# Optimization experiments

Hardware: AMD Instinct MI355X
Metric: run time of the kernel (lower is better)

## Reference

```python
import jax, jax.numpy as jnp
import numpy as np

P = 16           # patch size
D = 768          # embed / feature dim (= 3*P*P)
T = 8            # number of task vectors
H_META = 192     # MetaNet hidden (= D // 4)


def patchify(x):
    # x: [B, 3, H, W] -> [B, N, 3*P*P]
    B, C, H, W = x.shape
    x = x.reshape(B, C, H // P, P, W // P, P)
    x = x.transpose(0, 2, 4, 1, 3, 5)
    return x.reshape(B, (H // P) * (W // P), C * P * P)


def encode(W1, b1, W2, b2, x):
    # base functional encoder f(params, x): shared weights over the batch
    patches = patchify(x)                       # [B, N, D]
    h = jax.nn.relu(patches @ W1 + b1)          # [B, N, D]
    pooled = h.mean(axis=1)                     # [B, D]
    return pooled @ W2 + b2                     # [B, D]


def setup_inputs() -> dict:
    key = jax.random.key(0)
    ks = jax.random.split(key, 14)
    B = 64
    s = 0.02
    return {
        "x":   jax.random.normal(ks[0], (B, 3, 224, 224), jnp.float32),
        # base model params
        "W1":  jax.random.normal(ks[1], (D, D), jnp.float32) * s,
        "b1":  jax.random.normal(ks[2], (D,), jnp.float32) * s,
        "W2":  jax.random.normal(ks[3], (D, D), jnp.float32) * s,
        "b2":  jax.random.normal(ks[4], (D,), jnp.float32) * s,
        # task-vector deltas (stacked over T tasks)
        "dW1": jax.random.normal(ks[5], (T, D, D), jnp.float32) * s,
        "db1": jax.random.normal(ks[6], (T, D), jnp.float32) * s,
        "dW2": jax.random.normal(ks[7], (T, D, D), jnp.float32) * s,
        "db2": jax.random.normal(ks[8], (T, D), jnp.float32) * s,
        # MetaNet (Linear-ReLU-Linear); zero-init in the original, random here
        "mw1": jax.random.normal(ks[9], (D, H_META), jnp.float32) * s,
        "mb1": jax.random.normal(ks[10], (H_META,), jnp.float32) * s,
        "mw2": jax.random.normal(ks[11], (H_META, T), jnp.float32) * s,
        "mb2": jax.random.normal(ks[12], (T,), jnp.float32) * s,
    }


def reference(x, W1, b1, W2, b2, dW1, db1, dW2, db2, mw1, mb1, mw2, mb2):
    # 1) base features with frozen base model (torch.no_grad)
    base = jax.lax.stop_gradient(encode(W1, b1, W2, b2, x))       # [B, D]
    # 2) per-sample mixing coefficients via MetaNet
    coefs = jax.nn.relu(base @ mw1 + mb1) @ mw2 + mb2             # [B, T]
    # 3) per-sample mixed parameters: p + sum_t c[b,t] * dp[t]
    nW1 = W1 + jnp.einsum("bt,tij->bij", coefs, dW1)              # [B, D, D]
    nb1 = b1 + coefs @ db1                                        # [B, D]
    nW2 = W2 + jnp.einsum("bt,tij->bij", coefs, dW2)              # [B, D, D]
    nb2 = b2 + coefs @ db2                                        # [B, D]
    # 4) batched per-sample forward with the mixed weights
    patches = patchify(x)                                         # [B, N, D]
    h = jax.nn.relu(jnp.einsum("bnd,bde->bne", patches, nW1) + nb1[:, None, :])
    pooled = h.mean(axis=1)                                       # [B, D]
    out = jnp.einsum("bd,bde->be", pooled, nW2) + nb2             # [B, D]
    return out
```

## Files before the change

### kernel.cpp

```cpp
#include <hip/hip_runtime.h>
#include <hip/hip_bf16.h>


typedef __bf16 bf16x8 __attribute__((ext_vector_type(8)));
typedef float f32x4 __attribute__((ext_vector_type(4)));
typedef __hip_bfloat16 bf16;

struct alignas(16) BF8 { bf16 h[8]; };

constexpr int BATCH = 64;
constexpr int NP    = 196;
constexpr int NPAD  = 256;
constexpr int DIM   = 768;
constexpr int NT    = 8;
constexpr size_t MSZ = (size_t)DIM * DIM;

__device__ __forceinline__ void async_cp16(const void* g, void* l) {
  __builtin_amdgcn_global_load_lds(
      (const __attribute__((address_space(1))) uint32_t*)g,
      (__attribute__((address_space(3))) uint32_t*)l, 16, 0, 0);
}

__global__ void k_patchify(const float* __restrict__ x, bf16* __restrict__ A) {
  int idx  = blockIdx.x * blockDim.x + threadIdx.x;
  int col4 = idx % (DIM / 4);
  int row  = idx / (DIM / 4);
  int d = col4 * 4;
  int b = row >> 8;
  int n = row & 255;
  bf16 tmp[4];
  if (n < NP) {
    int hp = n / 14, wp = n % 14;
    int c  = d >> 8;
    int rr = d & 255;
    int i = rr >> 4, j = rr & 15;
    const float* src = x + ((((size_t)b * 3 + c) * 224 + hp * 16 + i) * 224 + wp * 16 + j);
    float4 f = *(const float4*)src;
    tmp[0] = __float2bfloat16(f.x);
    tmp[1] = __float2bfloat16(f.y);
    tmp[2] = __float2bfloat16(f.z);
    tmp[3] = __float2bfloat16(f.w);
  } else {
    tmp[0] = tmp[1] = tmp[2] = tmp[3] = __float2bfloat16(0.0f);
  }
  *(ushort4*)(A + (size_t)row * DIM + d) = *(ushort4*)tmp;
}

__global__ void k_transpose_cast(const float* __restrict__ W1, const float* __restrict__ dW1,
                                 const float* __restrict__ W2, const float* __restrict__ dW2,
                                 bf16* __restrict__ WT) {
  __shared__ float tile[32][33];
  int mat = blockIdx.z;
  const float* src;
  if      (mat == 0) src = W1;
  else if (mat <= 8) src = dW1 + (size_t)(mat - 1) * MSZ;
  else if (mat == 9) src = W2;
  else               src = dW2 + (size_t)(mat - 10) * MSZ;
  int n0 = blockIdx.x * 32;
  int k0 = blockIdx.y * 32;
  int tx = threadIdx.x & 31, ty = threadIdx.x >> 5;
#pragma unroll
  for (int r = ty; r < 32; r += 8)
    tile[r][tx] = src[(size_t)(k0 + r) * DIM + n0 + tx];
  __syncthreads();
  bf16* dst = WT + (size_t)mat * MSZ;
#pragma unroll
  for (int r = ty; r < 32; r += 8)
    dst[(size_t)(n0 + r) * DIM + k0 + tx] = __float2bfloat16(tile[tx][r]);
}


template<int MIX>
__global__ __launch_bounds__(256, 3)
void k_gemm_pool(const bf16* __restrict__ A,
                 const bf16* __restrict__ WT,
                 const float* __restrict__ b1,
                 const float* __restrict__ db1,
                 const float* __restrict__ coefs,
                 float* __restrict__ pooled) {
  __shared__ uint4 AslU[256 * 8];
  __shared__ uint4 BslU[64 * 8];
  __shared__ float biasl[64];
  __shared__ float cl[NT];
  __shared__ float red[4][64];

  int b  = blockIdx.x;
  int n0 = blockIdx.y * 64;
  int tid = threadIdx.x;

  if (MIX) {
    if (tid < NT) cl[tid] = coefs[b * NT + tid];
    __syncthreads();
  }
  if (tid < 64) {
    float bias = b1[n0 + tid];
    if (MIX) {
#pragma unroll
      for (int t = 0; t < NT; t++) bias += cl[t] * db1[t * DIM + n0 + tid];
    }
    biasl[tid] = bias;
  }
  float cr[NT];
  if (MIX) {
#pragma unroll
    for (int t = 0; t < NT; t++) cr[t] = cl[t];
  }

  const bf16* Ag = A + (size_t)b * NPAD * DIM;
  int wave = tid >> 6, lane = tid & 63;
  int quad = lane >> 4, l16 = lane & 15;
  f32x4 acc[4][4] = {};

  for (int kt = 0; kt < 12; kt++) {
    const bf16* Ak = Ag + kt * 64;
    const bf16* Wk = WT + kt * 64;
#pragma unroll
    for (int i = 0; i < 8; i++) {
      int s = wave * 512 + i * 64 + lane;
      int r = s >> 3, c = (s & 7) ^ (r & 7);
      async_cp16(Ak + (size_t)r * DIM + c * 8, (void*)(AslU + wave * 512 + i * 64));
    }
    if (!MIX) {
#pragma unroll
      for (int i = 0; i < 2; i++) {
        int s = wave * 128 + i * 64 + lane;
        int r = s >> 3, c = (s & 7) ^ (r & 7);
        async_cp16(Wk + (size_t)(n0 + r) * DIM + c * 8, (void*)(BslU + wave * 128 + i * 64));
      }
    } else {
#pragma unroll
      for (int i = 0; i < 2; i++) {
        int g = tid + 256 * i;
        int r = g >> 3, c = (g & 7) ^ (r & 7);
        const bf16* p0 = Wk + (size_t)(n0 + r) * DIM + c * 8;
        BF8 w = *(const BF8*)p0;
        float m[8];
#pragma unroll
        for (int j = 0; j < 8; j++) m[j] = __bfloat162float(w.h[j]);
#pragma unroll
        for (int t = 0; t < NT; t++) {
          BF8 dv = *(const BF8*)(p0 + (size_t)(1 + t) * MSZ);
          float cc = cr[t];
#pragma unroll
          for (int j = 0; j < 8; j++) m[j] += cc * __bfloat162float(dv.h[j]);
        }
        BF8 o;
#pragma unroll
        for (int j = 0; j < 8; j++) o.h[j] = __float2bfloat16(m[j]);
        BslU[g] = *(uint4*)&o;
      }
    }
    __syncthreads();
    const bf16* As = (const bf16*)AslU;
    const bf16* Bs = (const bf16*)BslU;
#pragma unroll
    for (int ks = 0; ks < 2; ks++) {
      bf16x8 bfr[4];
#pragma unroll
      for (int nf = 0; nf < 4; nf++) {
        int brow = nf * 16 + l16;
        bfr[nf] = *(const bf16x8*)(Bs + ((size_t)brow * 8 + ((ks * 4 + quad) ^ (brow & 7))) * 8);
      }
#pragma unroll
      for (int mf = 0; mf < 4; mf++) {
        int arow = wave * 64 + mf * 16 + l16;
        bf16x8 af = *(const bf16x8*)(As + ((size_t)arow * 8 + ((ks * 4 + quad) ^ (arow & 7))) * 8);
#pragma unroll
        for (int nf = 0; nf < 4; nf++)
          acc[mf][nf] = __builtin_amdgcn_mfma_f32_16x16x32_bf16(af, bfr[nf], acc[mf][nf], 0, 0, 0);
      }
    }
    __syncthreads();
  }

  int m0 = wave * 64;
  float colsum[4];
#pragma unroll
  for (int nf = 0; nf < 4; nf++) {
    float bias = biasl[nf * 16 + l16];
    float s = 0.0f;
#pragma unroll
    for (int mf = 0; mf < 4; mf++) {
      int rbase = m0 + mf * 16 + quad * 4;
#pragma unroll
      for (int r = 0; r < 4; r++) {
        if (rbase + r < NP) s += fmaxf(acc[mf][nf][r] + bias, 0.0f);
      }
    }
    s += __shfl_xor(s, 16, 64);
    s += __shfl_xor(s, 32, 64);
    colsum[nf] = s;
  }
  if (lane < 16) {
#pragma unroll
    for (int nf = 0; nf < 4; nf++) red[wave][nf * 16 + lane] = colsum[nf];
  }
  __syncthreads();
  if (tid < 64) {
    float s = red[0][tid] + red[1][tid] + red[2][tid] + red[3][tid];
    pooled[(size_t)b * DIM + n0 + tid] = s * (1.0f / 196.0f);
  }
}

__global__ __launch_bounds__(256, 2)
void k_gemm2(const float* __restrict__ Af,
             const bf16* __restrict__ WT,
             int matbase,
             const float* __restrict__ bias,
             float* __restrict__ Y) {
  __shared__ uint4 AslU[64 * 8];
  __shared__ uint4 BslU[64 * 8];
  int n0  = blockIdx.x * 64;
  int mat = blockIdx.y;
  int tid = threadIdx.x, wave = tid >> 6, lane = tid & 63;
  int quad = lane >> 4, l16 = lane & 15;
  f32x4 acc[4] = {};
  const bf16* Wm = WT + (size_t)(matbase + mat) * MSZ;
  for (int k0 = 0; k0 < DIM; k0 += 64) {
#pragma unroll
    for (int i = 0; i < 2; i++) {
      int g = tid + i * 256;
      int r = g >> 3, c = g & 7;
      const float* src = Af + (size_t)r * DIM + k0 + c * 8;
      float4 xa = ((const float4*)src)[0];
      float4 xb = ((const float4*)src)[1];
      BF8 o;
      o.h[0] = __float2bfloat16(xa.x); o.h[1] = __float2bfloat16(xa.y);
      o.h[2] = __float2bfloat16(xa.z); o.h[3] = __float2bfloat16(xa.w);
      o.h[4] = __float2bfloat16(xb.x); o.h[5] = __float2bfloat16(xb.y);
      o.h[6] = __float2bfloat16(xb.z); o.h[7] = __float2bfloat16(xb.w);
      AslU[r * 8 + (c ^ (r & 7))] = *(uint4*)&o;
      BslU[r * 8 + (c ^ (r & 7))] = *(const uint4*)(Wm + (size_t)(n0 + r) * DIM + k0 + c * 8);
    }
    __syncthreads();
    const bf16* As = (const bf16*)AslU;
    const bf16* Bs = (const bf16*)BslU;
#pragma unroll
    for (int ks = 0; ks < 2; ks++) {
      int brow = wave * 16 + l16;
      bf16x8 bfr = *(const bf16x8*)(Bs + (size_t)(brow * 8 + ((ks * 4 + quad) ^ (brow & 7))) * 8);
#pragma unroll
      for (int mf = 0; mf < 4; mf++) {
        int arow = mf * 16 + l16;
        bf16x8 af = *(const bf16x8*)(As + (size_t)(arow * 8 + ((ks * 4 + quad) ^ (arow & 7))) * 8);
        acc[mf] = __builtin_amdgcn_mfma_f32_16x16x32_bf16(af, bfr, acc[mf], 0, 0, 0);
      }
    }
    __syncthreads();
  }
#pragma unroll
  for (int mf = 0; mf < 4; mf++) {
#pragma unroll
    for (int r = 0; r < 4; r++) {
      int row = mf * 16 + quad * 4 + r;
      int col = n0 + wave * 16 + l16;
      float v = acc[mf][r];
      if (bias) v += bias[col];
      Y[((size_t)mat * 64 + row) * DIM + col] = v;
    }
  }
}

__global__ void k_metanet(const float* __restrict__ base,
                          const float* __restrict__ mw1, const float* __restrict__ mb1,
                          const float* __restrict__ mw2, const float* __restrict__ mb2,
                          float* __restrict__ coefs) {
  __shared__ float bl[DIM];
  __shared__ float hl[192];
  int b = blockIdx.x, tid = threadIdx.x;
  for (int i = tid; i < DIM; i += 192) bl[i] = base[(size_t)b * DIM + i];
  __syncthreads();
  float s = mb1[tid];
  for (int k = 0; k < DIM; k++) s += bl[k] * mw1[(size_t)k * 192 + tid];
  hl[tid] = fmaxf(s, 0.0f);
  __syncthreads();
  if (tid < NT) {
    float c = mb2[tid];
    for (int j = 0; j < 192; j++) c += hl[j] * mw2[(size_t)j * NT + tid];
    coefs[b * NT + tid] = c;
  }
}

__global__ void k_combine(const float* __restrict__ Y,
                          const float* __restrict__ coefs,
                          const float* __restrict__ b2,
                          const float* __restrict__ db2,
                          float* __restrict__ out) {
  int idx = blockIdx.x * 256 + threadIdx.x;
  int b = idx / DIM, e = idx % DIM;
  float v = Y[(size_t)b * DIM + e] + b2[e];
#pragma unroll
  for (int t = 0; t < NT; t++) {
    float c = coefs[b * NT + t];
    v += c * (Y[((size_t)(1 + t) * 64 + b) * DIM + e] + db2[(size_t)t * DIM + e]);
  }
  out[idx] = v;
}

extern "C" void kernel_launch(void* const* d_in, const int* in_sizes, int n_in,
                              void* d_out, int out_size, void* d_ws, size_t ws_size,
                              hipStream_t stream) {
  const float* x   = (const float*)d_in[0];
  const float* W1  = (const float*)d_in[1];
  const float* b1  = (const float*)d_in[2];
  const float* W2  = (const float*)d_in[3];
  const float* b2  = (const float*)d_in[4];
  const float* dW1 = (const float*)d_in[5];
  const float* db1 = (const float*)d_in[6];
  const float* dW2 = (const float*)d_in[7];
  const float* db2 = (const float*)d_in[8];
  const float* mw1 = (const float*)d_in[9];
  const float* mb1 = (const float*)d_in[10];
  const float* mw2 = (const float*)d_in[11];
  const float* mb2 = (const float*)d_in[12];
  float* out = (float*)d_out;
  (void)in_sizes; (void)n_in; (void)out_size; (void)ws_size;

  char* ws = (char*)d_ws;
  bf16*  A_bf    = (bf16*) (ws);
  bf16*  WT      = (bf16*) (ws + 25165824);
  float* pooledA = (float*)(ws + 46399488);
  float* pooledB = (float*)(ws + 46596096);
  float* coefs   = (float*)(ws + 46792704);
  float* base    = (float*)(ws + 46794752);
  float* Y       = (float*)(ws + 46991360);

  k_patchify<<<dim3((BATCH * NPAD * (DIM / 4)) / 256), 256, 0, stream>>>(x, A_bf);
  k_transpose_cast<<<dim3(24, 24, 18), 256, 0, stream>>>(W1, dW1, W2, dW2, WT);
  k_gemm_pool<0><<<dim3(BATCH, DIM / 64), 256, 0, stream>>>(A_bf, WT, b1, db1, nullptr, pooledA);
  k_gemm2<<<dim3(DIM / 64, 1), 256, 0, stream>>>(pooledA, WT, 9, b2, base);
  k_metanet<<<dim3(BATCH), 192, 0, stream>>>(base, mw1, mb1, mw2, mb2, coefs);
  k_gemm_pool<1><<<dim3(BATCH, DIM / 64), 256, 0, stream>>>(A_bf, WT, b1, db1, coefs, pooledB);
  k_gemm2<<<dim3(DIM / 64, 9), 256, 0, stream>>>(pooledB, WT, 9, nullptr, Y);
  k_combine<<<dim3((BATCH * DIM) / 256), 256, 0, stream>>>(Y, coefs, b2, db2, out);
}
```

Measured before the change: 306.6 us.

## Double-buffer LDS tiles in patch GEMM and skip padded rows beyond 224

Adds double buffering to the patch-embedding GEMM+pool kernel, so the next k-tile's A and B loads (async LDS copies, or register-staged mixed weights in the MIX path) are issued before the current tile's MFMAs run. It also loads only 224 of the 256 padded A rows and skips MFMAs for the all-padding row block. The bias is computed per lane at the end instead of being staged through LDS. The doubled LDS use and the larger register set for prefetched weights lower the occupancy target from 3 to 2 blocks per CU.

After: 293.9 us. 4.2% less time.

```diff
diff --git a/kernel.cpp b/kernel.cpp
--- a/kernel.cpp
+++ b/kernel.cpp
@@ -71,88 +71,97 @@
 
 
 template<int MIX>
-__global__ __launch_bounds__(256, 3)
+__global__ __launch_bounds__(256, 2)
 void k_gemm_pool(const bf16* __restrict__ A,
                  const bf16* __restrict__ WT,
                  const float* __restrict__ b1,
                  const float* __restrict__ db1,
                  const float* __restrict__ coefs,
                  float* __restrict__ pooled) {
-  __shared__ uint4 AslU[256 * 8];
-  __shared__ uint4 BslU[64 * 8];
-  __shared__ float biasl[64];
-  __shared__ float cl[NT];
-  __shared__ float red[4][64];
+  __shared__ uint4 AslU[2][1792];
+  __shared__ uint4 BslU[2][512];
 
   int b  = blockIdx.x;
   int n0 = blockIdx.y * 64;
   int tid = threadIdx.x;
-
-  if (MIX) {
-    if (tid < NT) cl[tid] = coefs[b * NT + tid];
-    __syncthreads();
-  }
-  if (tid < 64) {
-    float bias = b1[n0 + tid];
-    if (MIX) {
-#pragma unroll
-      for (int t = 0; t < NT; t++) bias += cl[t] * db1[t * DIM + n0 + tid];
-    }
-    biasl[tid] = bias;
-  }
+  int wave = tid >> 6, lane = tid & 63;
+  int quad = lane >> 4, l16 = lane & 15;
+
   float cr[NT];
   if (MIX) {
 #pragma unroll
-    for (int t = 0; t < NT; t++) cr[t] = cl[t];
+    for (int t = 0; t < NT; t++) cr[t] = coefs[b * NT + t];
   }
 
   const bf16* Ag = A + (size_t)b * NPAD * DIM;
-  int wave = tid >> 6, lane = tid & 63;
-  int quad = lane >> 4, l16 = lane & 15;
   f32x4 acc[4][4] = {};
 
+  auto stage_a = [&](int buf, int kt) {
+    const bf16* Ak = Ag + kt * 64;
+#pragma unroll
+    for (int i = 0; i < 7; i++) {
+      int s = (wave * 7 + i) * 64 + lane;
+      int r = s >> 3, c = (s & 7) ^ (r & 7);
+      async_cp16(Ak + (size_t)r * DIM + c * 8, (void*)&AslU[buf][(wave * 7 + i) * 64]);
+    }
+  };
+  auto stage_b_async = [&](int buf, int kt) {
+    const bf16* Wk = WT + kt * 64;
+#pragma unroll
+    for (int i = 0; i < 2; i++) {
+      int s = (wave * 2 + i) * 64 + lane;
+      int r = s >> 3, c = (s & 7) ^ (r & 7);
+      async_cp16(Wk + (size_t)(n0 + r) * DIM + c * 8, (void*)&BslU[buf][(wave * 2 + i) * 64]);
+    }
+  };
+  BF8 wreg[2][9];
+  auto mixb_load = [&](int kt) {
+    const bf16* Wk = WT + kt * 64;
+#pragma unroll
+    for (int i = 0; i < 2; i++) {
+      int g = tid + 256 * i;
+      int r = g >> 3, c = (g & 7) ^ (r & 7);
+      const bf16* p0 = Wk + (size_t)(n0 + r) * DIM + c * 8;
+      wreg[i][0] = *(const BF8*)p0;
+#pragma unroll
+      for (int t = 0; t < NT; t++)
+        wreg[i][1 + t] = *(const BF8*)(p0 + (size_t)(1 + t) * MSZ);
+    }
+  };
+  auto mixb_write = [&](int buf) {
+#pragma unroll
+    for (int i = 0; i < 2; i++) {
+      int g = tid + 256 * i;
+      float m[8];
+#pragma unroll
+      for (int j = 0; j < 8; j++) m[j] = __bfloat162float(wreg[i][0].h[j]);
+#pragma unroll
+      for (int t = 0; t < NT; t++) {
+        float cc = cr[t];
+#pragma unroll
+        for (int j = 0; j < 8; j++) m[j] += cc * __bfloat162float(wreg[i][1 + t].h[j]);
+      }
+      BF8 o;
+#pragma unroll
+      for (int j = 0; j < 8; j++) o.h[j] = __float2bfloat16(m[j]);
+      BslU[buf][g] = *(uint4*)&o;
+    }
+  };
+
+  stage_a(0, 0);
+  if (MIX) { mixb_load(0); mixb_write(0); }
+  else     stage_b_async(0, 0);
+  __syncthreads();
+
+  int cur = 0;
   for (int kt = 0; kt < 12; kt++) {
-    const bf16* Ak = Ag + kt * 64;
-    const bf16* Wk = WT + kt * 64;
-#pragma unroll
-    for (int i = 0; i < 8; i++) {
-      int s = wave * 512 + i * 64 + lane;
-      int r = s >> 3, c = (s & 7) ^ (r & 7);
-      async_cp16(Ak + (size_t)r * DIM + c * 8, (void*)(AslU + wave * 512 + i * 64));
-    }
-    if (!MIX) {
-#pragma unroll
-      for (int i = 0; i < 2; i++) {
-        int s = wave * 128 + i * 64 + lane;
-        int r = s >> 3, c = (s & 7) ^ (r & 7);
-        async_cp16(Wk + (size_t)(n0 + r) * DIM + c * 8, (void*)(BslU + wave * 128 + i * 64));
-      }
-    } else {
-#pragma unroll
-      for (int i = 0; i < 2; i++) {
-        int g = tid + 256 * i;
-        int r = g >> 3, c = (g & 7) ^ (r & 7);
-        const bf16* p0 = Wk + (size_t)(n0 + r) * DIM + c * 8;
-        BF8 w = *(const BF8*)p0;
-        float m[8];
-#pragma unroll
-        for (int j = 0; j < 8; j++) m[j] = __bfloat162float(w.h[j]);
-#pragma unroll
-        for (int t = 0; t < NT; t++) {
-          BF8 dv = *(const BF8*)(p0 + (size_t)(1 + t) * MSZ);
-          float cc = cr[t];
-#pragma unroll
-          for (int j = 0; j < 8; j++) m[j] += cc * __bfloat162float(dv.h[j]);
-        }
-        BF8 o;
-#pragma unroll
-        for (int j = 0; j < 8; j++) o.h[j] = __float2bfloat16(m[j]);
-        BslU[g] = *(uint4*)&o;
-      }
-    }
-    __syncthreads();
-    const bf16* As = (const bf16*)AslU;
-    const bf16* Bs = (const bf16*)BslU;
+    if (kt < 11) {
+      stage_a(cur ^ 1, kt + 1);
+      if (MIX) mixb_load(kt + 1);
+      else     stage_b_async(cur ^ 1, kt + 1);
+    }
+    const bf16* As = (const bf16*)AslU[cur];
+    const bf16* Bs = (const bf16*)BslU[cur];
 #pragma unroll
     for (int ks = 0; ks < 2; ks++) {
       bf16x8 bfr[4];
@@ -163,21 +172,31 @@
       }
 #pragma unroll
       for (int mf = 0; mf < 4; mf++) {
-        int arow = wave * 64 + mf * 16 + l16;
-        bf16x8 af = *(const bf16x8*)(As + ((size_t)arow * 8 + ((ks * 4 + quad) ^ (arow & 7))) * 8);
-#pragma unroll
-        for (int nf = 0; nf < 4; nf++)
-          acc[mf][nf] = __builtin_amdgcn_mfma_f32_16x16x32_bf16(af, bfr[nf], acc[mf][nf], 0, 0, 0);
-      }
-    }
+        if (wave * 64 + mf * 16 < 224) {
+          int arow = wave * 64 + mf * 16 + l16;
+          bf16x8 af = *(const bf16x8*)(As + ((size_t)arow * 8 + ((ks * 4 + quad) ^ (arow & 7))) * 8);
+#pragma unroll
+          for (int nf = 0; nf < 4; nf++)
+            acc[mf][nf] = __builtin_amdgcn_mfma_f32_16x16x32_bf16(af, bfr[nf], acc[mf][nf], 0, 0, 0);
+        }
+      }
+    }
+    if (MIX && kt < 11) mixb_write(cur ^ 1);
     __syncthreads();
-  }
-
+    cur ^= 1;
+  }
+
+  float* red = (float*)&BslU[0][0];
   int m0 = wave * 64;
   float colsum[4];
 #pragma unroll
   for (int nf = 0; nf < 4; nf++) {
-    float bias = biasl[nf * 16 + l16];
+    int col = n0 + nf * 16 + l16;
+    float bias = b1[col];
+    if (MIX) {
+#pragma unroll
+      for (int t = 0; t < NT; t++) bias += cr[t] * db1[t * DIM + col];
+    }
     float s = 0.0f;
 #pragma unroll
     for (int mf = 0; mf < 4; mf++) {
@@ -193,11 +212,11 @@
   }
   if (lane < 16) {
 #pragma unroll
-    for (int nf = 0; nf < 4; nf++) red[wave][nf * 16 + lane] = colsum[nf];
+    for (int nf = 0; nf < 4; nf++) red[wave * 64 + nf * 16 + lane] = colsum[nf];
   }
   __syncthreads();
   if (tid < 64) {
-    float s = red[0][tid] + red[1][tid] + red[2][tid] + red[3][tid];
+    float s = red[tid] + red[64 + tid] + red[128 + tid] + red[192 + tid];
     pooled[(size_t)b * DIM + n0 + tid] = s * (1.0f / 196.0f);
   }
 }
```
